# Kernel optimization log

Hardware: AMD Instinct MI355X
Metric: run time of the kernel (lower is better)

The kernel has to match this reference:

```python
import jax, jax.numpy as jnp
import numpy as np

P, T, UNITS = 256, 65536, 128
WIDTH = 1.0


def setup_inputs() -> dict:
    key = jax.random.key(0)
    k1, k2, k3 = jax.random.split(key, 3)
    inputs = jax.random.normal(k1, (P, T), dtype=jnp.float32)
    player_weights = jax.random.normal(k2, (P,), dtype=jnp.float32)
    kernel = jax.random.normal(k3, (T, UNITS), dtype=jnp.float32) * 0.01
    bias = jnp.zeros((UNITS,), dtype=jnp.float32)
    state = jnp.zeros((P,), dtype=jnp.float32)
    return {"inputs": inputs, "player_weights": player_weights,
            "kernel": kernel, "bias": bias, "state": state}


def _phi(x):
    # Phi(x) = max(x,0) + min(x+width,0)
    return jnp.maximum(x, 0.0) + jnp.minimum(x + WIDTH, 0.0)


def _play_scan(x_seq, s0):
    # sequential play-operator recurrence: s_t = Phi(w*x_t - s_{t-1}) + s_{t-1}
    def step(s, x):
        s_new = _phi(x - s) + s
        return s_new, s_new
    _, ys = jax.lax.scan(step, s0, x_seq)
    return ys  # [T]


def reference(inputs, player_weights, kernel, bias, state):
    scaled = inputs * player_weights[:, None]          # [P, T]
    outs = jax.vmap(_play_scan)(scaled, state)         # [P, T]
    y = outs @ kernel + bias                           # [P, units]
    return jnp.tanh(y)
```

## Files before the change

### kernel.cpp

```cpp
#include <hip/hip_runtime.h>
#include <math.h>

#define Pn 256
#define Tn 65536
#define Un 128
#define NC 512
#define CHUNK 128
#define ST 16

typedef float f4 __attribute__((ext_vector_type(4)));
typedef float f2 __attribute__((ext_vector_type(2)));


__global__ __launch_bounds__(1024) void kA(const float* __restrict__ in,
                                           const float* __restrict__ pw,
                                           f2* __restrict__ AB) {
  const int tid = threadIdx.x;
  const int W = blockIdx.x * 16 + (tid >> 6);
  const int l = tid & 63;
  const int c = W & (NC - 1);
  const int p = W >> 9;
  const float w = pw[p];
  f2 v = *(const f2*)(in + (size_t)p * Tn + (size_t)c * CHUNK + 2 * l);
  const float x0 = v.x * w, x1 = v.y * w;
  float A = fmaxf(x0, x1);
  float B = fminf(fmaxf(x0 + 1.0f, x1), x1 + 1.0f);
#pragma unroll
  for (int off = 1; off < 64; off <<= 1) {
    float A2 = __shfl_down(A, off);
    float B2 = __shfl_down(B, off);
    B = fminf(fmaxf(B, A2), B2);
    A = fmaxf(A, A2);
  }
  if (l == 0) {
    f2 r; r.x = A; r.y = B;
    AB[(size_t)p * NC + c] = r;
  }
}

__global__ __launch_bounds__(NC) void kB(const f2* __restrict__ AB,
                                         const float* __restrict__ st,
                                         float* __restrict__ sinb) {
  __shared__ float sA[NC], sB[NC];
  const int p = blockIdx.x;
  const int c = threadIdx.x;
  f2 ab = AB[(size_t)p * NC + c];
  sA[c] = ab.x;
  sB[c] = ab.y;
  __syncthreads();
#pragma unroll
  for (int d = 1; d < NC; d <<= 1) {
    float aL = 0.0f, bL = 0.0f;
    const bool has = (c >= d);
    if (has) { aL = sA[c - d]; bL = sB[c - d]; }
    __syncthreads();
    if (has) {
      float aS = sA[c], bS = sB[c];
      sB[c] = fminf(fmaxf(bL, aS), bS);
      sA[c] = fmaxf(aL, aS);
    }
    __syncthreads();
  }
  const float s0 = st[p];
  const float sin_c =
      (c == 0) ? s0 : fminf(fmaxf(s0, sA[c - 1]), sB[c - 1]);
  sinb[(size_t)c * Pn + p] = sin_c;
}

template <int CPG, bool ATOMIC>
__global__ __launch_bounds__(512, 4) void kC(const float* __restrict__ in,
                                             const float* __restrict__ pw,
                                             const float* __restrict__ Kg,
                                             const float* __restrict__ sinb,
                                             float* __restrict__ outp) {
  __shared__ float sS[2][ST][Pn];
  __shared__ float sK[2][ST][Un];
  const int tid = threadIdx.x;
  const int c0 = blockIdx.x * CPG;

  float w = 0.0f, s = 0.0f;
  const f4* src = nullptr;
  if (tid < Pn) {
    w = pw[tid];
    s = sinb[(size_t)c0 * Pn + tid];
    src = (const f4*)(in + (size_t)tid * Tn + (size_t)c0 * CHUNK);
  }

  const int ug = tid & 15, pg = tid >> 4;
  const int kr = tid >> 5, kcol = tid & 31;
  const f4* Kt = (const f4*)(Kg + (size_t)c0 * CHUNK * Un);

  float acc[2][4][2][4];
#pragma unroll
  for (int k1 = 0; k1 < 2; ++k1)
#pragma unroll
    for (int a = 0; a < 4; ++a)
#pragma unroll
      for (int k2 = 0; k2 < 2; ++k2)
#pragma unroll
        for (int l = 0; l < 4; ++l) acc[k1][a][k2][l] = 0.0f;

  const int nsub = (CHUNK * CPG) / ST;

  {
    f4 kv = Kt[kr * 32 + kcol];
    *(f4*)&sK[0][kr][kcol * 4] = kv;
    if (tid < Pn) {
#pragma unroll
      for (int i4 = 0; i4 < ST / 4; ++i4) {
        f4 v = src[i4];
#pragma unroll
        for (int j = 0; j < 4; ++j) {
          float x = v[j] * w;
          s = fminf(fmaxf(s, x), x + 1.0f);
          sS[0][i4 * 4 + j][tid] = s;
        }
      }
    }
  }
  __syncthreads();

  int b = 0;
  for (int sub = 0; sub < nsub; ++sub) {
    f4 kpre;
    f4 spre0, spre1, spre2, spre3;
    const bool more = (sub + 1 < nsub);
    if (more) {
      kpre = Kt[(sub + 1) * (ST * Un / 4) + kr * 32 + kcol];
      if (tid < Pn) {
        spre0 = src[(sub + 1) * (ST / 4) + 0];
        spre1 = src[(sub + 1) * (ST / 4) + 1];
        spre2 = src[(sub + 1) * (ST / 4) + 2];
        spre3 = src[(sub + 1) * (ST / 4) + 3];
      }
    }

    const float(*cs)[Pn] = sS[b];
    const float(*ck)[Un] = sK[b];
#pragma unroll 4
    for (int i = 0; i < ST; ++i) {
      f4 sv0 = *(const f4*)&cs[i][pg * 4];
      f4 sv1 = *(const f4*)&cs[i][128 + pg * 4];
      f4 kv0 = *(const f4*)&ck[i][ug * 4];
      f4 kv1 = *(const f4*)&ck[i][64 + ug * 4];
#pragma unroll
      for (int a = 0; a < 4; ++a) {
        float s0v = sv0[a], s1v = sv1[a];
#pragma unroll
        for (int l = 0; l < 4; ++l) {
          acc[0][a][0][l] += s0v * kv0[l];
          acc[0][a][1][l] += s0v * kv1[l];
          acc[1][a][0][l] += s1v * kv0[l];
          acc[1][a][1][l] += s1v * kv1[l];
        }
      }
    }

    if (more) {
      *(f4*)&sK[b ^ 1][kr][kcol * 4] = kpre;
      if (tid < Pn) {
        f4 pv[4] = {spre0, spre1, spre2, spre3};
#pragma unroll
        for (int i4 = 0; i4 < ST / 4; ++i4) {
#pragma unroll
          for (int j = 0; j < 4; ++j) {
            float x = pv[i4][j] * w;
            s = fminf(fmaxf(s, x), x + 1.0f);
            sS[b ^ 1][i4 * 4 + j][tid] = s;
          }
        }
      }
    }
    __syncthreads();
    b ^= 1;
  }

  if (ATOMIC) {
#pragma unroll
    for (int k1 = 0; k1 < 2; ++k1)
#pragma unroll
      for (int a = 0; a < 4; ++a) {
        int pp = k1 * 128 + pg * 4 + a;
#pragma unroll
        for (int k2 = 0; k2 < 2; ++k2)
#pragma unroll
          for (int l = 0; l < 4; ++l)
            atomicAdd(&outp[(size_t)pp * Un + k2 * 64 + ug * 4 + l],
                      acc[k1][a][k2][l]);
      }
  } else {
    float* base = outp + (size_t)blockIdx.x * (Pn * Un);
#pragma unroll
    for (int k1 = 0; k1 < 2; ++k1)
#pragma unroll
      for (int a = 0; a < 4; ++a) {
        int pp = k1 * 128 + pg * 4 + a;
#pragma unroll
        for (int k2 = 0; k2 < 2; ++k2) {
          f4 v;
#pragma unroll
          for (int l = 0; l < 4; ++l) v[l] = acc[k1][a][k2][l];
          *(f4*)&base[(size_t)pp * Un + k2 * 64 + ug * 4] = v;
        }
      }
  }
}

template <int NP>
__global__ __launch_bounds__(256) void kD(const float* __restrict__ part,
                                          const float* __restrict__ bias,
                                          float* __restrict__ out) {
  __shared__ float red[4][64];
  const int tid = threadIdx.x;
  const int o = tid & 63, qc = tid >> 6;
  const int g = blockIdx.x * 64 + o;
  float a = 0.0f;
#pragma unroll 4
  for (int k = 0; k < NP / 4; ++k)
    a += part[(size_t)(qc + 4 * k) * (Pn * Un) + g];
  red[qc][o] = a;
  __syncthreads();
  if (tid < 64) {
    float t = red[0][o] + red[1][o] + red[2][o] + red[3][o];
    out[g] = tanhf(t + bias[g & (Un - 1)]);
  }
}

__global__ __launch_bounds__(256) void kD2(float* __restrict__ out,
                                           const float* __restrict__ bias) {
  const int g = blockIdx.x * 256 + threadIdx.x;
  out[g] = tanhf(out[g] + bias[g & (Un - 1)]);
}

extern "C" void kernel_launch(void* const* d_in, const int* in_sizes, int n_in,
                              void* d_out, int out_size, void* d_ws,
                              size_t ws_size, hipStream_t stream) {
  const float* in   = (const float*)d_in[0];
  const float* pw   = (const float*)d_in[1];
  const float* Kg   = (const float*)d_in[2];
  const float* bias = (const float*)d_in[3];
  const float* st   = (const float*)d_in[4];
  float* out = (float*)d_out;
  float* wsf = (float*)d_ws;

  f2* AB      = (f2*)wsf;
  float* sinb = wsf + 2 * NC * Pn;
  float* part = wsf + 3 * NC * Pn;

  const size_t base_f = (size_t)3 * NC * Pn;
  const size_t need1 = (base_f + (size_t)NC * Pn * Un) * 4;
  const size_t need2 = (base_f + (size_t)(NC / 2) * Pn * Un) * 4;

  kA<<<(Pn * NC) / 16, 1024, 0, stream>>>(in, pw, AB);
  kB<<<Pn, NC, 0, stream>>>(AB, st, sinb);

  if (ws_size >= need1) {
    kC<1, false><<<NC, 512, 0, stream>>>(in, pw, Kg, sinb, part);
    kD<NC><<<(Pn * Un) / 64, 256, 0, stream>>>(part, bias, out);
  } else if (ws_size >= need2) {
    kC<2, false><<<NC / 2, 512, 0, stream>>>(in, pw, Kg, sinb, part);
    kD<NC / 2><<<(Pn * Un) / 64, 256, 0, stream>>>(part, bias, out);
  } else {
    hipMemsetAsync(out, 0, (size_t)Pn * Un * sizeof(float), stream);
    kC<2, true><<<NC / 2, 512, 0, stream>>>(in, pw, Kg, sinb, out);
    kD2<<<(Pn * Un) / 256, 256, 0, stream>>>(out, bias);
  }
}
```

Before: 201.4 us.

## Fuse chunk summary and prefix scan into one kernel, vectorize partial reduction

Replaces the separate per-chunk summary kernel and the shared-memory prefix-scan kernel with one kernel per player. In it, each of 1024 threads summarizes a 64-element segment serially, then does a wave-level shuffle scan and a 16-wave serial combine to produce the chunk entry states. This removes the AB intermediate buffer, one launch and the barrier-heavy log-step scan, in exchange for only 256 blocks and serial per-thread work. The final reduction kernel is rewritten to use float4 loads with 16-way splitting across 512 threads.

```diff
diff --git a/kernel.cpp b/kernel.cpp
--- a/kernel.cpp
+++ b/kernel.cpp
@@ -7,64 +7,62 @@
 #define NC 512
 #define CHUNK 128
 #define ST 16
+#define SEG 64
 
 typedef float f4 __attribute__((ext_vector_type(4)));
-typedef float f2 __attribute__((ext_vector_type(2)));
-
-
-__global__ __launch_bounds__(1024) void kA(const float* __restrict__ in,
-                                           const float* __restrict__ pw,
-                                           f2* __restrict__ AB) {
-  const int tid = threadIdx.x;
-  const int W = blockIdx.x * 16 + (tid >> 6);
-  const int l = tid & 63;
-  const int c = W & (NC - 1);
-  const int p = W >> 9;
-  const float w = pw[p];
-  f2 v = *(const f2*)(in + (size_t)p * Tn + (size_t)c * CHUNK + 2 * l);
-  const float x0 = v.x * w, x1 = v.y * w;
-  float A = fmaxf(x0, x1);
-  float B = fminf(fmaxf(x0 + 1.0f, x1), x1 + 1.0f);
+
+
+__global__ __launch_bounds__(1024) void kAB(const float* __restrict__ in,
+                                            const float* __restrict__ pw,
+                                            const float* __restrict__ st,
+                                            float* __restrict__ sinb) {
+  __shared__ float wA[16], wB[16], sw[16];
+  const int p = blockIdx.x;
+  const int t = threadIdx.x;
+  const int lane = t & 63, w = t >> 6;
+  const float wgt = pw[p];
+  const f4* src = (const f4*)(in + (size_t)p * Tn + (size_t)t * SEG);
+
+  float A = -3.402823466e38f, B = 3.402823466e38f;
+#pragma unroll
+  for (int i = 0; i < SEG / 4; ++i) {
+    f4 v = src[i];
+#pragma unroll
+    for (int j = 0; j < 4; ++j) {
+      float x = v[j] * wgt;
+      A = fmaxf(A, x);
+      B = fminf(fmaxf(B, x), x + 1.0f);
+    }
+  }
+
 #pragma unroll
   for (int off = 1; off < 64; off <<= 1) {
-    float A2 = __shfl_down(A, off);
-    float B2 = __shfl_down(B, off);
-    B = fminf(fmaxf(B, A2), B2);
-    A = fmaxf(A, A2);
-  }
-  if (l == 0) {
-    f2 r; r.x = A; r.y = B;
-    AB[(size_t)p * NC + c] = r;
-  }
-}
-
-__global__ __launch_bounds__(NC) void kB(const f2* __restrict__ AB,
-                                         const float* __restrict__ st,
-                                         float* __restrict__ sinb) {
-  __shared__ float sA[NC], sB[NC];
-  const int p = blockIdx.x;
-  const int c = threadIdx.x;
-  f2 ab = AB[(size_t)p * NC + c];
-  sA[c] = ab.x;
-  sB[c] = ab.y;
-  __syncthreads();
-#pragma unroll
-  for (int d = 1; d < NC; d <<= 1) {
-    float aL = 0.0f, bL = 0.0f;
-    const bool has = (c >= d);
-    if (has) { aL = sA[c - d]; bL = sB[c - d]; }
-    __syncthreads();
-    if (has) {
-      float aS = sA[c], bS = sB[c];
-      sB[c] = fminf(fmaxf(bL, aS), bS);
-      sA[c] = fmaxf(aL, aS);
-    }
-    __syncthreads();
-  }
-  const float s0 = st[p];
-  const float sin_c =
-      (c == 0) ? s0 : fminf(fmaxf(s0, sA[c - 1]), sB[c - 1]);
-  sinb[(size_t)c * Pn + p] = sin_c;
+    float Ar = __shfl_up(A, off);
+    float Br = __shfl_up(B, off);
+    if (lane >= off) {
+      B = fminf(fmaxf(Br, A), B);
+      A = fmaxf(Ar, A);
+    }
+  }
+  if (lane == 63) { wA[w] = A; wB[w] = B; }
+  __syncthreads();
+
+  if (t == 0) {
+    float s = st[p];
+#pragma unroll
+    for (int q = 0; q < 16; ++q) {
+      sw[q] = s;
+      s = fminf(fmaxf(s, wA[q]), wB[q]);
+    }
+  }
+  __syncthreads();
+
+  float Ae = __shfl_up(A, 1);
+  float Be = __shfl_up(B, 1);
+  float s_in = (lane == 0) ? sw[w] : fminf(fmaxf(sw[w], Ae), Be);
+
+  if ((t & 1) == 0)
+    sinb[(size_t)(t >> 1) * Pn + p] = s_in;
 }
 
 template <int CPG, bool ATOMIC>
@@ -207,22 +205,38 @@
 }
 
 template <int NP>
-__global__ __launch_bounds__(256) void kD(const float* __restrict__ part,
+__global__ __launch_bounds__(512) void kD(const float* __restrict__ part,
                                           const float* __restrict__ bias,
                                           float* __restrict__ out) {
-  __shared__ float red[4][64];
+  __shared__ f4 red[16][33];
   const int tid = threadIdx.x;
-  const int o = tid & 63, qc = tid >> 6;
-  const int g = blockIdx.x * 64 + o;
-  float a = 0.0f;
-#pragma unroll 4
-  for (int k = 0; k < NP / 4; ++k)
-    a += part[(size_t)(qc + 4 * k) * (Pn * Un) + g];
-  red[qc][o] = a;
-  __syncthreads();
-  if (tid < 64) {
-    float t = red[0][o] + red[1][o] + red[2][o] + red[3][o];
-    out[g] = tanhf(t + bias[g & (Un - 1)]);
+  const int fg = tid & 31, qc = tid >> 5;
+  constexpr int PG = NP / 16;
+  const f4* p4 = (const f4*)part;
+  const size_t g4 = (size_t)blockIdx.x * 32 + fg;
+
+  f4 acc = {0.0f, 0.0f, 0.0f, 0.0f};
+  for (int k = 0; k < PG; ++k) {
+    f4 v = p4[(size_t)(qc * PG + k) * (Pn * Un / 4) + g4];
+    acc.x += v.x; acc.y += v.y; acc.z += v.z; acc.w += v.w;
+  }
+  red[qc][fg] = acc;
+  __syncthreads();
+
+  if (tid < 32) {
+    f4 s = red[0][fg];
+#pragma unroll
+    for (int q = 1; q < 16; ++q) {
+      f4 v = red[q][fg];
+      s.x += v.x; s.y += v.y; s.z += v.z; s.w += v.w;
+    }
+    f4 bv = ((const f4*)bias)[fg];
+    f4 o;
+    o.x = tanhf(s.x + bv.x);
+    o.y = tanhf(s.y + bv.y);
+    o.z = tanhf(s.z + bv.z);
+    o.w = tanhf(s.w + bv.w);
+    ((f4*)out)[g4] = o;
   }
 }
 
@@ -243,23 +257,21 @@
   float* out = (float*)d_out;
   float* wsf = (float*)d_ws;
 
-  f2* AB      = (f2*)wsf;
-  float* sinb = wsf + 2 * NC * Pn;
-  float* part = wsf + 3 * NC * Pn;
-
-  const size_t base_f = (size_t)3 * NC * Pn;
+  float* sinb = wsf;
+  float* part = wsf + NC * Pn;
+
+  const size_t base_f = (size_t)NC * Pn;
   const size_t need1 = (base_f + (size_t)NC * Pn * Un) * 4;
   const size_t need2 = (base_f + (size_t)(NC / 2) * Pn * Un) * 4;
 
-  kA<<<(Pn * NC) / 16, 1024, 0, stream>>>(in, pw, AB);
-  kB<<<Pn, NC, 0, stream>>>(AB, st, sinb);
+  kAB<<<Pn, 1024, 0, stream>>>(in, pw, st, sinb);
 
   if (ws_size >= need1) {
     kC<1, false><<<NC, 512, 0, stream>>>(in, pw, Kg, sinb, part);
-    kD<NC><<<(Pn * Un) / 64, 256, 0, stream>>>(part, bias, out);
+    kD<NC><<<(Pn * Un / 4) / 32, 512, 0, stream>>>(part, bias, out);
   } else if (ws_size >= need2) {
     kC<2, false><<<NC / 2, 512, 0, stream>>>(in, pw, Kg, sinb, part);
-    kD<NC / 2><<<(Pn * Un) / 64, 256, 0, stream>>>(part, bias, out);
+    kD<NC / 2><<<(Pn * Un / 4) / 32, 512, 0, stream>>>(part, bias, out);
   } else {
     hipMemsetAsync(out, 0, (size_t)Pn * Un * sizeof(float), stream);
     kC<2, true><<<NC / 2, 512, 0, stream>>>(in, pw, Kg, sinb, out);
```

New measurement: 189.7 us. 1.06x faster.
